# Performance work log

Hardware: AMD Instinct MI355X
Metric: run time of the kernel (lower is better)

## Reference

```python
import jax, jax.numpy as jnp
import numpy as np

GAMMA = 0.99
GAE_LAMBDA = 0.95
CLIP = 0.2
ENT_COEF = 0.01
VF_COEF = 0.5


def setup_inputs() -> dict:
    key = jax.random.key(0)
    ks = jax.random.split(key, 12)
    T, D, H, A = 65536, 512, 256, 16
    obs = jax.random.normal(ks[0], (T, D), dtype=jnp.float32)
    actions = jax.random.randint(ks[1], (T,), 0, A, dtype=jnp.int32)
    logprobs = jax.random.normal(ks[2], (T,), dtype=jnp.float32)
    rewards = jax.random.normal(ks[3], (T,), dtype=jnp.float32)
    terms = jax.random.uniform(ks[4], (T,), dtype=jnp.float32)
    values = jax.random.normal(ks[5], (T,), dtype=jnp.float32)
    # orthogonal-init-like scaling (std sqrt(2) for trunk, 0.01 actor, 1.0 critic)
    W1 = jax.random.normal(ks[6], (D, H), dtype=jnp.float32) * np.float32(np.sqrt(2.0 / D))
    b1 = jnp.zeros((H,), jnp.float32)
    W2 = jax.random.normal(ks[7], (H, H), dtype=jnp.float32) * np.float32(np.sqrt(2.0 / H))
    b2 = jnp.zeros((H,), jnp.float32)
    Wa = jax.random.normal(ks[8], (H, A), dtype=jnp.float32) * np.float32(0.01 / np.sqrt(H))
    ba = jnp.zeros((A,), jnp.float32)
    Wc = jax.random.normal(ks[9], (H, 1), dtype=jnp.float32) * np.float32(1.0 / np.sqrt(H))
    bc = jnp.zeros((1,), jnp.float32)
    return {"obs": obs, "actions": actions, "logprobs": logprobs, "rewards": rewards,
            "terms": terms, "values": values, "W1": W1, "b1": b1, "W2": W2, "b2": b2,
            "Wa": Wa, "ba": ba, "Wc": Wc, "bc": bc}


def reference(obs, actions, logprobs, rewards, terms, values,
              W1, b1, W2, b2, Wa, ba, Wc, bc):
    # ---- GAE (torch.no_grad in original -> stop_gradient) ----
    nonterm = 1.0 - terms                                   # [T]
    next_vals = jnp.concatenate([values[1:], jnp.zeros((1,), values.dtype)])
    delta = rewards + GAMMA * next_vals * nonterm - values  # [T]

    def step(carry, x):  # reverse recurrence a_t = d_t + g*l*nt_t * a_{t+1}
        d, nt = x
        g = d + GAMMA * GAE_LAMBDA * nt * carry
        return g, g

    _, adv = jax.lax.scan(step, jnp.float32(0.0), (delta, nonterm), reverse=True)
    adv = jax.lax.stop_gradient(adv)
    returns = adv + jax.lax.stop_gradient(values)
    vals_old = jax.lax.stop_gradient(values)

    # ---- actor-critic MLP (get_action_and_value) ----
    hidden = jnp.tanh(jnp.tanh(obs @ W1 + b1) @ W2 + b2)    # [T,256]
    logits = hidden @ Wa + ba                               # [T,A]
    logp = jax.nn.log_softmax(logits, axis=-1)
    newlp = jnp.take_along_axis(logp, actions[:, None].astype(jnp.int32), axis=1)[:, 0]
    entropy = -jnp.sum(jnp.exp(logp) * logp, axis=-1)       # [T]
    value = (hidden @ Wc + bc)[:, 0]                        # [T]

    # ---- clipped PPO losses (single full-batch minibatch) ----
    ratio = jnp.exp(newlp - logprobs)
    a = (adv - adv.mean()) / (adv.std() + 1e-8)
    pg_loss = jnp.maximum(-a * ratio, -a * jnp.clip(ratio, 1.0 - CLIP, 1.0 + CLIP)).mean()
    v_clipped = vals_old + jnp.clip(value - vals_old, -CLIP, CLIP)
    v_loss = 0.5 * jnp.maximum((value - returns) ** 2, (v_clipped - returns) ** 2).mean()
    loss = pg_loss - ENT_COEF * entropy.mean() + VF_COEF * v_loss
    return loss
```

## Files before the change

kernel.cpp:

```cpp
#include <hip/hip_runtime.h>


#define TT 65536

typedef float f32x4 __attribute__((ext_vector_type(4)));
typedef __bf16 bf16x8 __attribute__((ext_vector_type(8)));
typedef unsigned short u16x8 __attribute__((ext_vector_type(8)));
typedef unsigned int u32x4 __attribute__((ext_vector_type(4)));

__device__ __forceinline__ unsigned short f2bf(float f) {
    unsigned int u = __float_as_uint(f);
    unsigned int r = (u + 0x7fffu + ((u >> 16) & 1u)) >> 16;
    return (unsigned short)r;
}

__device__ __forceinline__ unsigned int cvt_pk_bf16(float a, float b) {
    unsigned int r;
    asm volatile("v_cvt_pk_bf16_f32 %0, %1, %2" : "=v"(r) : "v"(a), "v"(b));
    return r;
}

__device__ __forceinline__ float fast_tanh(float x) {
    float e = __expf(2.0f * x);
    return fmaf(-2.0f, __builtin_amdgcn_rcpf(e + 1.0f), 1.0f);
}

__device__ __forceinline__ void async_lds16(void* lds, const void* g) {
    __builtin_amdgcn_global_load_lds(
        (const __attribute__((address_space(1))) unsigned int*)g,
        (__attribute__((address_space(3))) unsigned int*)lds, 16, 0, 0);
}

__device__ __forceinline__ void suffix_scan256(float* sC, float* sD, int i) {
    float c = sC[i], d = sD[i];
#pragma unroll
    for (int s = 1; s < 256; s <<= 1) {
        float c2 = 1.0f, d2 = 0.0f;
        if (i + s < 256) { c2 = sC[i + s]; d2 = sD[i + s]; }
        __syncthreads();
        d = d + c * d2;
        c = c * c2;
        sC[i] = c; sD[i] = d;
        __syncthreads();
    }
}

__device__ __forceinline__ void gae_cd(const float* rewards, const float* terms,
                                       const float* values, int t, float* c, float* d) {
    float nt = 1.0f - terms[t];
    float nv = (t + 1 < TT) ? values[t + 1] : 0.0f;
    *d = rewards[t] + 0.99f * nv * nt - values[t];
    *c = 0.99f * 0.95f * nt;
}

__global__ void k_prep_gae1(const float* __restrict__ W1, const float* __restrict__ W2,
                            const float* __restrict__ Wa, const float* __restrict__ Wc,
                            unsigned short* __restrict__ W1T, unsigned short* __restrict__ W2T,
                            unsigned short* __restrict__ WavT,
                            const float* __restrict__ rewards, const float* __restrict__ terms,
                            const float* __restrict__ values, float* __restrict__ aggC,
                            float* __restrict__ aggD) {
    if (blockIdx.x < 800) {
        int idx = blockIdx.x * 256 + threadIdx.x;
        if (idx < 131072) {
            int kt = idx >> 13;
            int L = (idx & 8191) >> 3, e = idx & 7;
            int row = L >> 2, p = L & 3;
            int k = kt * 32 + (((p ^ ((row >> 1) & 3)) << 3) | e);
            W1T[idx] = f2bf(W1[k * 256 + row]);
        } else if (idx < 196608) {
            int i = idx - 131072;
            int kt = i >> 13;
            int L = (i & 8191) >> 3, e = i & 7;
            int row = L >> 2, p = L & 3;
            int k = kt * 32 + (((p ^ ((row >> 1) & 3)) << 3) | e);
            W2T[i] = f2bf(W2[k * 256 + row]);
        } else if (idx < 204800) {
            int i = idx - 196608;
            int L = i >> 3, e = i & 7;
            int row = L >> 5, ec = (L & 31) << 3;
            int k = ((ec ^ ((row & 7) << 3)) | e);
            float v = (row < 16) ? Wa[k * 16 + row] : ((row == 16) ? Wc[k] : 0.0f);
            WavT[i] = f2bf(v);
        }
        return;
    }
    __shared__ float sC[256], sD[256];
    int i = threadIdx.x;
    int b = blockIdx.x - 800;
    int t = b * 256 + i;
    float c, d;
    gae_cd(rewards, terms, values, t, &c, &d);
    sC[i] = c; sD[i] = d;
    __syncthreads();
    suffix_scan256(sC, sD, i);
    if (i == 0) { aggC[b] = sC[0]; aggD[b] = sD[0]; }
}

__global__ void k_gae3(const float* __restrict__ rewards, const float* __restrict__ terms,
                       const float* __restrict__ values, const float* __restrict__ aggC,
                       const float* __restrict__ aggD, float* __restrict__ adv,
                       float* __restrict__ ret, float* __restrict__ sumP) {
    __shared__ float sC[256], sD[256];
    int i = threadIdx.x, b = blockIdx.x;
    sC[i] = aggC[i]; sD[i] = aggD[i];
    __syncthreads();
    suffix_scan256(sC, sD, i);
    float carry = (b < 255) ? sD[b + 1] : 0.0f;
    __syncthreads();

    int t = b * 256 + i;
    float c, d;
    gae_cd(rewards, terms, values, t, &c, &d);
    sC[i] = c; sD[i] = d;
    __syncthreads();
    suffix_scan256(sC, sD, i);
    float a = sD[i] + sC[i] * carry;
    adv[t] = a;
    ret[t] = a + values[t];
    __syncthreads();
    sC[i] = a; sD[i] = a * a;
    __syncthreads();
#pragma unroll
    for (int s = 128; s > 0; s >>= 1) {
        if (i < s) { sC[i] += sC[i + s]; sD[i] += sD[i + s]; }
        __syncthreads();
    }
    if (i == 0) { sumP[2 * b] = sC[0]; sumP[2 * b + 1] = sD[0]; }
}

__global__ void k_gae4(const float* __restrict__ sumP, float* __restrict__ stats) {
    __shared__ float s1[256], s2[256];
    int i = threadIdx.x;
    s1[i] = sumP[2 * i]; s2[i] = sumP[2 * i + 1];
    __syncthreads();
#pragma unroll
    for (int s = 128; s > 0; s >>= 1) {
        if (i < s) { s1[i] += s1[i + s]; s2[i] += s2[i + s]; }
        __syncthreads();
    }
    if (i == 0) {
        float mean = s1[0] * (1.0f / TT);
        float var = s2[0] * (1.0f / TT) - mean * mean;
        stats[0] = mean;
        stats[1] = 1.0f / (sqrtf(fmaxf(var, 0.0f)) + 1e-8f);
    }
}

__global__ __launch_bounds__(256, 3) void k_mlp(
    const float* __restrict__ obs, const int* __restrict__ actions,
    const float* __restrict__ logprobs, const float* __restrict__ values,
    const float* __restrict__ b1, const float* __restrict__ b2,
    const float* __restrict__ ba, const float* __restrict__ bc,
    const unsigned short* __restrict__ W1T, const unsigned short* __restrict__ W2T,
    const unsigned short* __restrict__ WavT, const float* __restrict__ adv,
    const float* __restrict__ ret, const float* __restrict__ stats,
    float* __restrict__ lossP) {
    __shared__ __align__(16) unsigned char SM[49152];
    unsigned short* smB1 = (unsigned short*)SM;
    unsigned short* smA  = (unsigned short*)(SM + 32768);
    unsigned short* smH  = (unsigned short*)SM;
    unsigned short* smB2 = (unsigned short*)(SM + 32768);

    const int tid = threadIdx.x;
    const int wid = tid >> 6;
    const int lane = tid & 63;
    const int cl = lane & 15;
    const int gg = lane >> 4;
    const int bm0 = blockIdx.x * 64;

    const int arow = tid >> 2;
    const int aslot = tid & 3;
    const int adst = arow * 32 + ((aslot ^ ((arow >> 1) & 3)) << 3);
    const float* aSrc = obs + (size_t)(bm0 + arow) * 512 + aslot * 8;

    const float meanA = stats[0], rstdA = stats[1];

    float b1v[4], b2v[4];
#pragma unroll
    for (int n = 0; n < 4; ++n) {
        int c = wid * 64 + n * 16 + cl;
        b1v[n] = b1[c];
        b2v[n] = b2[c];
    }
    const float bav = ba[cl];
    const float bc0 = bc[0];

    f32x4 acc[4][4];
#pragma unroll
    for (int m = 0; m < 4; ++m)
#pragma unroll
        for (int n = 0; n < 4; ++n) acc[m][n] = (f32x4){0.f, 0.f, 0.f, 0.f};

    auto stageTile = [&](const unsigned short* src, unsigned short* dst) {
#pragma unroll
        for (int c = 0; c < 4; ++c) {
            int chunk = wid * 4 + c;
            async_lds16(dst + chunk * 512, src + chunk * 512 + lane * 8);
        }
    };
    auto cvtWriteA = [&](const float4& f0, const float4& f1, int buf) {
        u32x4 pk;
        pk[0] = cvt_pk_bf16(f0.x, f0.y);
        pk[1] = cvt_pk_bf16(f0.z, f0.w);
        pk[2] = cvt_pk_bf16(f1.x, f1.y);
        pk[3] = cvt_pk_bf16(f1.z, f1.w);
        *(u32x4*)&smA[buf * 2048 + adst] = pk;
    };

    {
        float4 a0 = *(const float4*)(aSrc);
        float4 a1 = *(const float4*)(aSrc + 4);
        stageTile(W1T, smB1);
        cvtWriteA(a0, a1, 0);
        __syncthreads();
#pragma unroll
        for (int t = 0; t < 16; ++t) {
            if (t < 15) {
                a0 = *(const float4*)(aSrc + (t + 1) * 32);
                a1 = *(const float4*)(aSrc + (t + 1) * 32 + 4);
                stageTile(W1T + (t + 1) * 8192, smB1 + ((t + 1) & 1) * 8192);
            }
            bf16x8 av[4], bv[4];
#pragma unroll
            for (int m = 0; m < 4; ++m) {
                int ra = m * 16 + cl;
                av[m] = *(const bf16x8*)&smA[(t & 1) * 2048 + ra * 32 + ((gg ^ ((ra >> 1) & 3)) << 3)];
            }
#pragma unroll
            for (int n = 0; n < 4; ++n) {
                int rb = wid * 64 + n * 16 + cl;
                bv[n] = *(const bf16x8*)&smB1[(t & 1) * 8192 + rb * 32 + ((gg ^ ((rb >> 1) & 3)) << 3)];
            }
#pragma unroll
            for (int m = 0; m < 4; ++m)
#pragma unroll
                for (int n = 0; n < 4; ++n)
                    acc[m][n] = __builtin_amdgcn_mfma_f32_16x16x32_bf16(av[m], bv[n], acc[m][n], 0, 0, 0);
            if (t < 15) cvtWriteA(a0, a1, (t + 1) & 1);
            __syncthreads();
        }
    }

    stageTile(W2T, smB2);
#pragma unroll
    for (int m = 0; m < 4; ++m)
#pragma unroll
        for (int n = 0; n < 4; ++n)
#pragma unroll
            for (int jp = 0; jp < 2; ++jp) {
                float v0 = fast_tanh(acc[m][n][2 * jp] + b1v[n]);
                float v1 = fast_tanh(acc[m][n][2 * jp + 1] + b1v[n]);
                unsigned int p = cvt_pk_bf16(v0, v1);
                int r0 = m * 16 + gg * 4 + 2 * jp;
                int c = wid * 64 + n * 16 + cl;
                smH[r0 * 256 + (c ^ ((r0 & 7) << 3))] = (unsigned short)p;
                int r1 = r0 + 1;
                smH[r1 * 256 + (c ^ ((r1 & 7) << 3))] = (unsigned short)(p >> 16);
                acc[m][n][2 * jp] = 0.0f;
                acc[m][n][2 * jp + 1] = 0.0f;
            }
    __syncthreads();

#pragma unroll
    for (int t = 0; t < 8; ++t) {
        bf16x8 av[4], bv[4];
#pragma unroll
        for (int m = 0; m < 4; ++m) {
            int ra = m * 16 + cl;
            av[m] = *(const bf16x8*)&smH[ra * 256 + ((t * 32 + gg * 8) ^ ((ra & 7) << 3))];
        }
#pragma unroll
        for (int n = 0; n < 4; ++n) {
            int rb = wid * 64 + n * 16 + cl;
            bv[n] = *(const bf16x8*)&smB2[rb * 32 + ((gg ^ ((rb >> 1) & 3)) << 3)];
        }
#pragma unroll
        for (int m = 0; m < 4; ++m)
#pragma unroll
            for (int n = 0; n < 4; ++n)
                acc[m][n] = __builtin_amdgcn_mfma_f32_16x16x32_bf16(av[m], bv[n], acc[m][n], 0, 0, 0);
        __syncthreads();
        if (t < 7) stageTile(W2T + (t + 1) * 8192, smB2);
        else       stageTile(WavT, smB2);
        __syncthreads();
    }

#pragma unroll
    for (int m = 0; m < 4; ++m)
#pragma unroll
        for (int n = 0; n < 4; ++n)
#pragma unroll
            for (int jp = 0; jp < 2; ++jp) {
                float v0 = fast_tanh(acc[m][n][2 * jp] + b2v[n]);
                float v1 = fast_tanh(acc[m][n][2 * jp + 1] + b2v[n]);
                unsigned int p = cvt_pk_bf16(v0, v1);
                int r0 = m * 16 + gg * 4 + 2 * jp;
                int c = wid * 64 + n * 16 + cl;
                smH[r0 * 256 + (c ^ ((r0 & 7) << 3))] = (unsigned short)p;
                int r1 = r0 + 1;
                smH[r1 * 256 + (c ^ ((r1 & 7) << 3))] = (unsigned short)(p >> 16);
            }
    __syncthreads();

    float lsum = 0.0f;
    {
        f32x4 acc_a = {0.f, 0.f, 0.f, 0.f}, acc_v = {0.f, 0.f, 0.f, 0.f};
#pragma unroll
        for (int kk = 0; kk < 8; ++kk) {
            int r = wid * 16 + cl;
            bf16x8 av = *(const bf16x8*)&smH[r * 256 + ((kk * 32 + gg * 8) ^ ((r & 7) << 3))];
            int ra2 = cl;
            bf16x8 bva = *(const bf16x8*)&smB2[ra2 * 256 + ((kk * 32 + gg * 8) ^ ((ra2 & 7) << 3))];
            int rv = 16 + cl;
            bf16x8 bvv = *(const bf16x8*)&smB2[rv * 256 + ((kk * 32 + gg * 8) ^ ((rv & 7) << 3))];
            acc_a = __builtin_amdgcn_mfma_f32_16x16x32_bf16(av, bva, acc_a, 0, 0, 0);
            acc_v = __builtin_amdgcn_mfma_f32_16x16x32_bf16(av, bvv, acc_v, 0, 0, 0);
        }

        const int t0 = bm0 + wid * 16;
#pragma unroll
        for (int j = 0; j < 4; ++j) {
            int t = t0 + gg * 4 + j;
            float lg = acc_a[j] + bav;
            float mx = lg;
#pragma unroll
            for (int dd = 1; dd < 16; dd <<= 1) mx = fmaxf(mx, __shfl_xor(mx, dd));
            float ex = __expf(lg - mx);
            float se = ex;
#pragma unroll
            for (int dd = 1; dd < 16; dd <<= 1) se += __shfl_xor(se, dd);
            float ls = __logf(se);
            float lp = lg - mx - ls;
            float pl = __expf(lp) * lp;
            float ent = pl;
#pragma unroll
            for (int dd = 1; dd < 16; dd <<= 1) ent += __shfl_xor(ent, dd);
            ent = -ent;
            int act = actions[t];
            float newlp = __shfl(lp, (lane & 48) | act);
            float val = __shfl(acc_v[j], lane & 48) + bc0;

            float lpo = logprobs[t];
            float at = (adv[t] - meanA) * rstdA;
            float rt = ret[t];
            float vo = values[t];
            float ratio = __expf(newlp - lpo);
            float rcl = fminf(fmaxf(ratio, 0.8f), 1.2f);
            float pg = fmaxf(-at * ratio, -at * rcl);
            float vcl = vo + fminf(fmaxf(val - vo, -0.2f), 0.2f);
            float dv = val - rt, dvc = vcl - rt;
            float vl = fmaxf(dv * dv, dvc * dvc);
            if (cl == 0) lsum += pg - 0.01f * ent + 0.25f * vl;
        }
        lsum += __shfl_xor(lsum, 16);
        lsum += __shfl_xor(lsum, 32);
    }
    __syncthreads();
    float* red2 = (float*)SM;
    if (lane == 0) red2[wid] = lsum;
    __syncthreads();
    if (tid == 0) lossP[blockIdx.x] = red2[0] + red2[1] + red2[2] + red2[3];
}

__global__ void k_final(const float* __restrict__ lossP, float* __restrict__ out) {
    __shared__ float s[256];
    int i = threadIdx.x;
    s[i] = lossP[i] + lossP[i + 256] + lossP[i + 512] + lossP[i + 768];
    __syncthreads();
#pragma unroll
    for (int st = 128; st > 0; st >>= 1) {
        if (i < st) s[i] += s[i + st];
        __syncthreads();
    }
    if (i == 0) out[0] = s[0] * (1.0f / TT);
}

extern "C" void kernel_launch(void* const* d_in, const int* in_sizes, int n_in,
                              void* d_out, int out_size, void* d_ws, size_t ws_size,
                              hipStream_t stream) {
    const float* obs      = (const float*)d_in[0];
    const int*   actions  = (const int*)d_in[1];
    const float* logprobs = (const float*)d_in[2];
    const float* rewards  = (const float*)d_in[3];
    const float* terms    = (const float*)d_in[4];
    const float* values   = (const float*)d_in[5];
    const float* W1 = (const float*)d_in[6];
    const float* b1 = (const float*)d_in[7];
    const float* W2 = (const float*)d_in[8];
    const float* b2 = (const float*)d_in[9];
    const float* Wa = (const float*)d_in[10];
    const float* ba = (const float*)d_in[11];
    const float* Wc = (const float*)d_in[12];
    const float* bc = (const float*)d_in[13];

    char* ws = (char*)d_ws;
    unsigned short* W1T  = (unsigned short*)(ws + 0);
    unsigned short* W2T  = (unsigned short*)(ws + 262144);
    unsigned short* WavT = (unsigned short*)(ws + 393216);
    float* advp  = (float*)(ws + 409600);
    float* retp  = (float*)(ws + 671744);
    float* aggC  = (float*)(ws + 933888);
    float* aggD  = (float*)(ws + 934912);
    float* sumP  = (float*)(ws + 936960);
    float* stats = (float*)(ws + 939008);
    float* lossP = (float*)(ws + 939072);

    k_prep_gae1<<<1056, 256, 0, stream>>>(W1, W2, Wa, Wc, W1T, W2T, WavT,
                                          rewards, terms, values, aggC, aggD);
    k_gae3<<<256, 256, 0, stream>>>(rewards, terms, values, aggC, aggD, advp, retp, sumP);
    k_gae4<<<1, 256, 0, stream>>>(sumP, stats);
    k_mlp<<<1024, 256, 0, stream>>>(obs, actions, logprobs, values, b1, b2, ba, bc,
                                    W1T, W2T, WavT, advp, retp, stats, lossP);
    k_final<<<1, 256, 0, stream>>>(lossP, (float*)d_out);
}
```

Before: 75.87 us.

## Load MFMA weight fragments directly from global instead of staging via LDS

The prep kernel now lays out W1, W2 and the actor/critic weights in MFMA fragment order, so each lane reads its bf16x8 B operand straight from global memory (L2-resident) instead of async-copying tiles into LDS. This removes the LDS staging, the weight double buffer and many __syncthreads in the layer-2 loop, and shrinks LDS from 48KB to 40KB. In exchange every MFMA step now waits on global/L2 load latency with no explicit prefetch, and the tanh outputs are written as single bf16 scalars instead of packed pairs.

```diff
diff --git a/kernel.cpp b/kernel.cpp
--- a/kernel.cpp
+++ b/kernel.cpp
@@ -16,19 +16,13 @@
 
 __device__ __forceinline__ unsigned int cvt_pk_bf16(float a, float b) {
     unsigned int r;
-    asm volatile("v_cvt_pk_bf16_f32 %0, %1, %2" : "=v"(r) : "v"(a), "v"(b));
+    asm("v_cvt_pk_bf16_f32 %0, %1, %2" : "=v"(r) : "v"(a), "v"(b));
     return r;
 }
 
 __device__ __forceinline__ float fast_tanh(float x) {
     float e = __expf(2.0f * x);
     return fmaf(-2.0f, __builtin_amdgcn_rcpf(e + 1.0f), 1.0f);
-}
-
-__device__ __forceinline__ void async_lds16(void* lds, const void* g) {
-    __builtin_amdgcn_global_load_lds(
-        (const __attribute__((address_space(1))) unsigned int*)g,
-        (__attribute__((address_space(3))) unsigned int*)lds, 16, 0, 0);
 }
 
 __device__ __forceinline__ void suffix_scan256(float* sC, float* sD, int i) {
@@ -55,33 +49,31 @@
 
 __global__ void k_prep_gae1(const float* __restrict__ W1, const float* __restrict__ W2,
                             const float* __restrict__ Wa, const float* __restrict__ Wc,
-                            unsigned short* __restrict__ W1T, unsigned short* __restrict__ W2T,
-                            unsigned short* __restrict__ WavT,
+                            unsigned short* __restrict__ W1Tf, unsigned short* __restrict__ W2Tf,
+                            unsigned short* __restrict__ Wavf,
                             const float* __restrict__ rewards, const float* __restrict__ terms,
                             const float* __restrict__ values, float* __restrict__ aggC,
                             float* __restrict__ aggD) {
     if (blockIdx.x < 800) {
         int idx = blockIdx.x * 256 + threadIdx.x;
         if (idx < 131072) {
-            int kt = idx >> 13;
-            int L = (idx & 8191) >> 3, e = idx & 7;
-            int row = L >> 2, p = L & 3;
-            int k = kt * 32 + (((p ^ ((row >> 1) & 3)) << 3) | e);
-            W1T[idx] = f2bf(W1[k * 256 + row]);
+            int e = idx & 7, l = (idx >> 3) & 63, nt = (idx >> 9) & 15, kt = idx >> 13;
+            int col = nt * 16 + (l & 15);
+            int k = kt * 32 + ((l >> 4) << 3) + e;
+            W1Tf[idx] = f2bf(W1[k * 256 + col]);
         } else if (idx < 196608) {
             int i = idx - 131072;
-            int kt = i >> 13;
-            int L = (i & 8191) >> 3, e = i & 7;
-            int row = L >> 2, p = L & 3;
-            int k = kt * 32 + (((p ^ ((row >> 1) & 3)) << 3) | e);
-            W2T[i] = f2bf(W2[k * 256 + row]);
+            int e = i & 7, l = (i >> 3) & 63, nt = (i >> 9) & 15, kt = i >> 13;
+            int col = nt * 16 + (l & 15);
+            int k = kt * 32 + ((l >> 4) << 3) + e;
+            W2Tf[i] = f2bf(W2[k * 256 + col]);
         } else if (idx < 204800) {
             int i = idx - 196608;
-            int L = i >> 3, e = i & 7;
-            int row = L >> 5, ec = (L & 31) << 3;
-            int k = ((ec ^ ((row & 7) << 3)) | e);
-            float v = (row < 16) ? Wa[k * 16 + row] : ((row == 16) ? Wc[k] : 0.0f);
-            WavT[i] = f2bf(v);
+            int e = i & 7, l = (i >> 3) & 63, h = (i >> 9) & 1, kt = i >> 10;
+            int k = kt * 32 + ((l >> 4) << 3) + e;
+            int a = l & 15;
+            float v = (h == 0) ? Wa[k * 16 + a] : ((a == 0) ? Wc[k] : 0.0f);
+            Wavf[i] = f2bf(v);
         }
         return;
     }
@@ -152,15 +144,13 @@
     const float* __restrict__ logprobs, const float* __restrict__ values,
     const float* __restrict__ b1, const float* __restrict__ b2,
     const float* __restrict__ ba, const float* __restrict__ bc,
-    const unsigned short* __restrict__ W1T, const unsigned short* __restrict__ W2T,
-    const unsigned short* __restrict__ WavT, const float* __restrict__ adv,
+    const unsigned short* __restrict__ W1Tf, const unsigned short* __restrict__ W2Tf,
+    const unsigned short* __restrict__ Wavf, const float* __restrict__ adv,
     const float* __restrict__ ret, const float* __restrict__ stats,
     float* __restrict__ lossP) {
-    __shared__ __align__(16) unsigned char SM[49152];
-    unsigned short* smB1 = (unsigned short*)SM;
-    unsigned short* smA  = (unsigned short*)(SM + 32768);
-    unsigned short* smH  = (unsigned short*)SM;
-    unsigned short* smB2 = (unsigned short*)(SM + 32768);
+    __shared__ __align__(16) unsigned char SM[40960];
+    unsigned short* smA = (unsigned short*)SM;
+    unsigned short* smH = (unsigned short*)(SM + 8192);
 
     const int tid = threadIdx.x;
     const int wid = tid >> 6;
@@ -192,13 +182,6 @@
 #pragma unroll
         for (int n = 0; n < 4; ++n) acc[m][n] = (f32x4){0.f, 0.f, 0.f, 0.f};
 
-    auto stageTile = [&](const unsigned short* src, unsigned short* dst) {
-#pragma unroll
-        for (int c = 0; c < 4; ++c) {
-            int chunk = wid * 4 + c;
-            async_lds16(dst + chunk * 512, src + chunk * 512 + lane * 8);
-        }
-    };
     auto cvtWriteA = [&](const float4& f0, const float4& f1, int buf) {
         u32x4 pk;
         pk[0] = cvt_pk_bf16(f0.x, f0.y);
@@ -209,9 +192,9 @@
     };
 
     {
+        const unsigned short* bBase = W1Tf + ((size_t)(wid * 4) << 9) + lane * 8;
         float4 a0 = *(const float4*)(aSrc);
         float4 a1 = *(const float4*)(aSrc + 4);
-        stageTile(W1T, smB1);
         cvtWriteA(a0, a1, 0);
         __syncthreads();
 #pragma unroll
@@ -219,18 +202,15 @@
             if (t < 15) {
                 a0 = *(const float4*)(aSrc + (t + 1) * 32);
                 a1 = *(const float4*)(aSrc + (t + 1) * 32 + 4);
-                stageTile(W1T + (t + 1) * 8192, smB1 + ((t + 1) & 1) * 8192);
             }
             bf16x8 av[4], bv[4];
+#pragma unroll
+            for (int n = 0; n < 4; ++n)
+                bv[n] = *(const bf16x8*)(bBase + ((size_t)(t * 16 + n) << 9));
 #pragma unroll
             for (int m = 0; m < 4; ++m) {
                 int ra = m * 16 + cl;
                 av[m] = *(const bf16x8*)&smA[(t & 1) * 2048 + ra * 32 + ((gg ^ ((ra >> 1) & 3)) << 3)];
-            }
-#pragma unroll
-            for (int n = 0; n < 4; ++n) {
-                int rb = wid * 64 + n * 16 + cl;
-                bv[n] = *(const bf16x8*)&smB1[(t & 1) * 8192 + rb * 32 + ((gg ^ ((rb >> 1) & 3)) << 3)];
             }
 #pragma unroll
             for (int m = 0; m < 4; ++m)
@@ -242,78 +222,63 @@
         }
     }
 
-    stageTile(W2T, smB2);
 #pragma unroll
     for (int m = 0; m < 4; ++m)
 #pragma unroll
         for (int n = 0; n < 4; ++n)
 #pragma unroll
-            for (int jp = 0; jp < 2; ++jp) {
-                float v0 = fast_tanh(acc[m][n][2 * jp] + b1v[n]);
-                float v1 = fast_tanh(acc[m][n][2 * jp + 1] + b1v[n]);
-                unsigned int p = cvt_pk_bf16(v0, v1);
-                int r0 = m * 16 + gg * 4 + 2 * jp;
+            for (int j = 0; j < 4; ++j) {
+                int r = m * 16 + gg * 4 + j;
                 int c = wid * 64 + n * 16 + cl;
-                smH[r0 * 256 + (c ^ ((r0 & 7) << 3))] = (unsigned short)p;
-                int r1 = r0 + 1;
-                smH[r1 * 256 + (c ^ ((r1 & 7) << 3))] = (unsigned short)(p >> 16);
-                acc[m][n][2 * jp] = 0.0f;
-                acc[m][n][2 * jp + 1] = 0.0f;
-            }
-    __syncthreads();
-
-#pragma unroll
-    for (int t = 0; t < 8; ++t) {
-        bf16x8 av[4], bv[4];
-#pragma unroll
-        for (int m = 0; m < 4; ++m) {
-            int ra = m * 16 + cl;
-            av[m] = *(const bf16x8*)&smH[ra * 256 + ((t * 32 + gg * 8) ^ ((ra & 7) << 3))];
-        }
-#pragma unroll
-        for (int n = 0; n < 4; ++n) {
-            int rb = wid * 64 + n * 16 + cl;
-            bv[n] = *(const bf16x8*)&smB2[rb * 32 + ((gg ^ ((rb >> 1) & 3)) << 3)];
-        }
-#pragma unroll
-        for (int m = 0; m < 4; ++m)
+                smH[r * 256 + (c ^ ((r & 7) << 3))] = f2bf(fast_tanh(acc[m][n][j] + b1v[n]));
+                acc[m][n][j] = 0.0f;
+            }
+    __syncthreads();
+
+    {
+        const unsigned short* bBase = W2Tf + ((size_t)(wid * 4) << 9) + lane * 8;
+#pragma unroll
+        for (int t = 0; t < 8; ++t) {
+            bf16x8 av[4], bv[4];
 #pragma unroll
             for (int n = 0; n < 4; ++n)
-                acc[m][n] = __builtin_amdgcn_mfma_f32_16x16x32_bf16(av[m], bv[n], acc[m][n], 0, 0, 0);
-        __syncthreads();
-        if (t < 7) stageTile(W2T + (t + 1) * 8192, smB2);
-        else       stageTile(WavT, smB2);
-        __syncthreads();
-    }
-
+                bv[n] = *(const bf16x8*)(bBase + ((size_t)(t * 16 + n) << 9));
+#pragma unroll
+            for (int m = 0; m < 4; ++m) {
+                int ra = m * 16 + cl;
+                av[m] = *(const bf16x8*)&smH[ra * 256 + ((t * 32 + gg * 8) ^ ((ra & 7) << 3))];
+            }
+#pragma unroll
+            for (int m = 0; m < 4; ++m)
+#pragma unroll
+                for (int n = 0; n < 4; ++n)
+                    acc[m][n] = __builtin_amdgcn_mfma_f32_16x16x32_bf16(av[m], bv[n], acc[m][n], 0, 0, 0);
+        }
+    }
+
+    __syncthreads();
 #pragma unroll
     for (int m = 0; m < 4; ++m)
 #pragma unroll
         for (int n = 0; n < 4; ++n)
 #pragma unroll
-            for (int jp = 0; jp < 2; ++jp) {
-                float v0 = fast_tanh(acc[m][n][2 * jp] + b2v[n]);
-                float v1 = fast_tanh(acc[m][n][2 * jp + 1] + b2v[n]);
-                unsigned int p = cvt_pk_bf16(v0, v1);
-                int r0 = m * 16 + gg * 4 + 2 * jp;
+            for (int j = 0; j < 4; ++j) {
+                int r = m * 16 + gg * 4 + j;
                 int c = wid * 64 + n * 16 + cl;
-                smH[r0 * 256 + (c ^ ((r0 & 7) << 3))] = (unsigned short)p;
-                int r1 = r0 + 1;
-                smH[r1 * 256 + (c ^ ((r1 & 7) << 3))] = (unsigned short)(p >> 16);
+                smH[r * 256 + (c ^ ((r & 7) << 3))] = f2bf(fast_tanh(acc[m][n][j] + b2v[n]));
             }
     __syncthreads();
 
     float lsum = 0.0f;
     {
         f32x4 acc_a = {0.f, 0.f, 0.f, 0.f}, acc_v = {0.f, 0.f, 0.f, 0.f};
+        const unsigned short* wBase = Wavf + lane * 8;
 #pragma unroll
         for (int kk = 0; kk < 8; ++kk) {
             int r = wid * 16 + cl;
             bf16x8 av = *(const bf16x8*)&smH[r * 256 + ((kk * 32 + gg * 8) ^ ((r & 7) << 3))];
-            int ra2 = cl;
-            bf16x8 bva = *(const bf16x8*)&smB2[ra2 * 256 + ((kk * 32 + gg * 8) ^ ((ra2 & 7) << 3))];
-            int rv = 16 + cl;
-            bf16x8 bvv = *(const bf16x8*)&smB2[rv * 256 + ((kk * 32 + gg * 8) ^ ((rv & 7) << 3))];
+            bf16x8 bva = *(const bf16x8*)(wBase + ((size_t)(kk * 2) << 9));
+            bf16x8 bvv = *(const bf16x8*)(wBase + ((size_t)(kk * 2 + 1) << 9));
             acc_a = __builtin_amdgcn_mfma_f32_16x16x32_bf16(av, bva, acc_a, 0, 0, 0);
             acc_v = __builtin_amdgcn_mfma_f32_16x16x32_bf16(av, bvv, acc_v, 0, 0, 0);
         }
@@ -395,9 +360,9 @@
     const float* bc = (const float*)d_in[13];
 
     char* ws = (char*)d_ws;
-    unsigned short* W1T  = (unsigned short*)(ws + 0);
-    unsigned short* W2T  = (unsigned short*)(ws + 262144);
-    unsigned short* WavT = (unsigned short*)(ws + 393216);
+    unsigned short* W1Tf = (unsigned short*)(ws + 0);
+    unsigned short* W2Tf = (unsigned short*)(ws + 262144);
+    unsigned short* Wavf = (unsigned short*)(ws + 393216);
     float* advp  = (float*)(ws + 409600);
     float* retp  = (float*)(ws + 671744);
     float* aggC  = (float*)(ws + 933888);
@@ -406,11 +371,11 @@
     float* stats = (float*)(ws + 939008);
     float* lossP = (float*)(ws + 939072);
 
-    k_prep_gae1<<<1056, 256, 0, stream>>>(W1, W2, Wa, Wc, W1T, W2T, WavT,
+    k_prep_gae1<<<1056, 256, 0, stream>>>(W1, W2, Wa, Wc, W1Tf, W2Tf, Wavf,
                                           rewards, terms, values, aggC, aggD);
     k_gae3<<<256, 256, 0, stream>>>(rewards, terms, values, aggC, aggD, advp, retp, sumP);
     k_gae4<<<1, 256, 0, stream>>>(sumP, stats);
     k_mlp<<<1024, 256, 0, stream>>>(obs, actions, logprobs, values, b1, b2, ba, bc,
-                                    W1T, W2T, WavT, advp, retp, stats, lossP);
+                                    W1Tf, W2Tf, Wavf, advp, retp, stats, lossP);
     k_final<<<1, 256, 0, stream>>>(lossP, (float*)d_out);
 }
```

Measured after the change: 66.54 us. 1.14x faster.
